# Optimization experiments

Hardware: AMD Instinct MI355X
Metric: run time of the kernel (lower is better)

Reference implementation:

```python
import jax, jax.numpy as jnp
import numpy as np

N_NODES = 50000
N_EDGES = 600000
D = 128
EDGE_DIM = 1
N_LAYERS = 2
NEG_SLOPE = 0.2


def setup_inputs() -> dict:
    key = jax.random.key(0)
    ks = jax.random.split(key, 8)
    x = jax.random.normal(ks[0], (N_NODES, D), dtype=jnp.float32)
    edge_index = jax.random.randint(ks[1], (2, N_EDGES), 0, N_NODES, dtype=jnp.int64)
    edge_attr = jax.random.normal(ks[2], (N_EDGES, EDGE_DIM), dtype=jnp.float32)
    s = 1.0 / np.sqrt(D)
    Wl = jax.random.normal(ks[3], (N_LAYERS, D, D), dtype=jnp.float32) * s   # lin_l weights
    Wr = jax.random.normal(ks[4], (N_LAYERS, D, D), dtype=jnp.float32) * s   # lin_r weights
    We = jax.random.normal(ks[5], (N_LAYERS, EDGE_DIM, D), dtype=jnp.float32) * s  # lin_edge
    att = jax.random.normal(ks[6], (N_LAYERS, D), dtype=jnp.float32) * s     # attention vector (heads=1)
    bias = jnp.zeros((N_LAYERS, D), dtype=jnp.float32)
    return {"x": x, "edge_index": edge_index, "edge_attr": edge_attr,
            "Wl": Wl, "Wr": Wr, "We": We, "att": att, "bias": bias}


def _gatv2_layer(x, src, dst, edge_attr, Wl, Wr, We, att, bias):
    # GATv2Conv, heads=1, add_self_loops=False, share_weights=False.
    xl = x @ Wl                                   # [N, D] (source transform)
    xr = x @ Wr                                   # [N, D] (target transform)
    m = xl[src] + xr[dst] + edge_attr @ We        # [E, D]
    m = jax.nn.leaky_relu(m, NEG_SLOPE)
    logits = m @ att                              # [E]
    # segment softmax over incoming edges of each dst node
    mx = jax.ops.segment_max(logits, dst, num_segments=N_NODES)  # [N]
    ex = jnp.exp(logits - mx[dst])                # [E]
    denom = jax.ops.segment_sum(ex, dst, num_segments=N_NODES)   # [N]
    alpha = ex / jnp.maximum(denom[dst], 1e-16)   # [E]
    out = jax.ops.segment_sum(alpha[:, None] * xl[src], dst, num_segments=N_NODES)
    return out + bias


def reference(x, edge_index, edge_attr, Wl, Wr, We, att, bias):
    src, dst = edge_index[0], edge_index[1]
    h = x
    for l in range(N_LAYERS):
        h = _gatv2_layer(h, src, dst, edge_attr, Wl[l], Wr[l], We[l], att[l], bias[l])
        h = jax.nn.relu(h)   # activation; norm=None, dropout=0 (eval) are identity
    return h
```

## Files before the change

### kernel.cpp

```cpp
#include <hip/hip_runtime.h>
#include <hip/hip_fp16.h>

#define N_NODES 50000
#define N_PAD   50048
#define N_EDGES 600000
#define DD 128
#define NEG_SLOPE 0.2f
#define BSHIFT 7
#define NBUCKETS 391
#define MAXB 2048

typedef _Float16 h2 __attribute__((ext_vector_type(2)));
typedef _Float16 h8 __attribute__((ext_vector_type(8)));
typedef __attribute__((ext_vector_type(4))) float f32x4;
typedef unsigned long long u64;

__device__ inline h2 bch2(unsigned u) { return __builtin_bit_cast(h2, u); }
__device__ inline unsigned h2u(h2 h) { return __builtin_bit_cast(unsigned, h); }
__device__ inline ushort f2h_bits(float x) {
    return __builtin_bit_cast(ushort, (_Float16)x);
}

#if __has_builtin(__builtin_amdgcn_fdot2)
#define DOT2(a, b, c) __builtin_amdgcn_fdot2((a), (b), (c), false)
#else
#define DOT2(a, b, c) ((c) + (float)(a)[0] * (float)(b)[0] + (float)(a)[1] * (float)(b)[1])
#endif

__global__ void pack_detect(const float* __restrict__ Wl, const float* __restrict__ Wr,
                            ushort* __restrict__ Wp,
                            const int* __restrict__ ei, int* __restrict__ flag,
                            int* __restrict__ bcount) {
    if (blockIdx.x == 256) {
        for (int t = threadIdx.x; t < NBUCKETS; t += 256) bcount[t] = 0;
        if (threadIdx.x == 0) {
            int is64 = 1;
            for (int i = 0; i < 64; ++i) {
                if (ei[2 * i + 1] != 0) { is64 = 0; break; }
            }
            *flag = is64;
        }
        return;
    }
    int idx = blockIdx.x * 256 + threadIdx.x;
    int layer = idx >> 15;
    int which = (idx >> 14) & 1;
    int kk    = (idx >> 12) & 3;
    int c     = (idx >> 9) & 7;
    int lane  = (idx >> 3) & 63;
    int j     = idx & 7;
    int k   = kk * 32 + (lane >> 4) * 8 + j;
    int col = c * 16 + (lane & 15);
    const float* W = which ? Wr : Wl;
    Wp[idx] = f2h_bits(W[(size_t)layer * DD * DD + k * DD + col]);
}

__global__ __launch_bounds__(512) void bin_edges(
    const int* __restrict__ ei, const int* __restrict__ flag,
    const float* __restrict__ ea, int* __restrict__ bcount,
    u64* __restrict__ tmp) {
    __shared__ int lhist[NBUCKETS];
    __shared__ int lbase[NBUCKETS];
    for (int i = threadIdx.x; i < NBUCKETS; i += 512) lhist[i] = 0;
    __syncthreads();
    const bool is64 = (*flag) != 0;
    int base = blockIdx.x * 4096;
    int myb[8], myrank[8];
    u64 mypack[8];
    #pragma unroll
    for (int i = 0; i < 8; ++i) {
        int e = base + i * 512 + threadIdx.x;
        if (e < N_EDGES) {
            int s, d;
            if (is64) {
                const long long* e64 = (const long long*)ei;
                s = (int)e64[e];
                d = (int)e64[N_EDGES + e];
            } else {
                s = ei[e];
                d = ei[N_EDGES + e];
            }
            unsigned hb = (unsigned)f2h_bits(ea[e]);
            int b = d >> BSHIFT;
            myb[i] = b;
            mypack[i] = ((u64)(unsigned)(d & 127) << 32) | ((u64)hb << 16) | (unsigned)s;
            myrank[i] = atomicAdd(&lhist[b], 1);
        } else myb[i] = -1;
    }
    __syncthreads();
    for (int i = threadIdx.x; i < NBUCKETS; i += 512) {
        int c = lhist[i];
        lbase[i] = c ? atomicAdd(&bcount[i], c) : 0;
    }
    __syncthreads();
    #pragma unroll
    for (int i = 0; i < 8; ++i)
        if (myb[i] >= 0) {
            int rel = lbase[myb[i]] + myrank[i];
            if (rel < MAXB)
                tmp[(size_t)myb[i] * MAXB + rel] = mypack[i];
        }
}

__global__ __launch_bounds__(256) void scatter_sort(
    const u64* __restrict__ tmp, const int* __restrict__ bcount,
    unsigned* __restrict__ se_csr, int* __restrict__ row_start) {
    __shared__ int bscan[512];
    __shared__ int lcnt[128];
    __shared__ int lscan[128];
    __shared__ int lcur[128];
    int tid = threadIdx.x;
    {
        int v = 0;
        if (tid < NBUCKETS) { v = bcount[tid]; if (v > MAXB) v = MAXB; }
        bscan[tid] = v;
        int v2 = 0;
        if (tid + 256 < NBUCKETS) { v2 = bcount[tid + 256]; if (v2 > MAXB) v2 = MAXB; }
        bscan[tid + 256] = v2;
    }
    __syncthreads();
    #pragma unroll
    for (int off = 1; off < 512; off <<= 1) {
        int t0 = (tid >= off) ? bscan[tid - off] : 0;
        int t1 = (tid + 256 >= off) ? bscan[tid + 256 - off] : 0;
        __syncthreads();
        bscan[tid] += t0;
        bscan[tid + 256] += t1;
        __syncthreads();
    }
    int b = blockIdx.x;
    int boff = (b == 0) ? 0 : bscan[b - 1];
    if (b == 0 && tid == 0) row_start[N_NODES] = bscan[NBUCKETS - 1];

    if (tid < 128) lcnt[tid] = 0;
    __syncthreads();
    int n_e = bcount[b]; if (n_e > MAXB) n_e = MAXB;
    const u64* tb = tmp + (size_t)b * MAXB;
    for (int e = tid; e < n_e; e += 256)
        atomicAdd(&lcnt[(int)(tb[e] >> 32)], 1);
    __syncthreads();
    if (tid < 128) lscan[tid] = lcnt[tid];
    __syncthreads();
    #pragma unroll
    for (int off = 1; off < 128; off <<= 1) {
        int t = 0;
        if (tid < 128 && tid >= off) t = lscan[tid - off];
        __syncthreads();
        if (tid < 128) lscan[tid] += t;
        __syncthreads();
    }
    int nb = b << BSHIFT;
    if (tid < 128) {
        int start = boff + lscan[tid] - lcnt[tid];
        lcur[tid] = start;
        if (nb + tid < N_NODES) row_start[nb + tid] = start;
    }
    __syncthreads();
    for (int e = tid; e < n_e; e += 256) {
        u64 w = tb[e];
        int pos = atomicAdd(&lcur[(int)(w >> 32)], 1);
        se_csr[pos] = (unsigned)w;
    }
}

template<bool AF32>
__global__ __launch_bounds__(256) void gemm_mfma(
    const ushort* __restrict__ h, const float* __restrict__ xf,
    const ushort* __restrict__ Wp,
    ushort* __restrict__ xl, ushort* __restrict__ xr) {
    __shared__ ushort wlds[32768];
    #pragma unroll
    for (int i = 0; i < 16; ++i) {
        int idx = i * 256 + threadIdx.x;
        ((uint4*)wlds)[idx] = ((const uint4*)Wp)[idx];
    }
    int wave = threadIdx.x >> 6, lane = threadIdx.x & 63;
    int arow = blockIdx.x * 64 + wave * 16 + (lane & 15);
    int kbase = (lane >> 4) * 8;
    f32x4 accl[8], accr[8];
    #pragma unroll
    for (int c = 0; c < 8; ++c) {
        accl[c] = (f32x4){0.f, 0.f, 0.f, 0.f};
        accr[c] = (f32x4){0.f, 0.f, 0.f, 0.f};
    }
    __syncthreads();
    #pragma unroll
    for (int kk = 0; kk < 4; ++kk) {
        h8 a;
        if (AF32) {
            if (arow < N_NODES) {
                const float* xp = xf + (size_t)arow * DD + kk * 32 + kbase;
                float4 u0 = *(const float4*)xp;
                float4 u1 = *(const float4*)(xp + 4);
                a[0] = (_Float16)u0.x; a[1] = (_Float16)u0.y;
                a[2] = (_Float16)u0.z; a[3] = (_Float16)u0.w;
                a[4] = (_Float16)u1.x; a[5] = (_Float16)u1.y;
                a[6] = (_Float16)u1.z; a[7] = (_Float16)u1.w;
            } else {
                #pragma unroll
                for (int i = 0; i < 8; ++i) a[i] = (_Float16)0.f;
            }
        } else {
            a = *(const h8*)&h[(size_t)arow * DD + kk * 32 + kbase];
        }
        #pragma unroll
        for (int c = 0; c < 8; ++c) {
            h8 bl = *(const h8*)&wlds[((kk * 8 + c) * 64 + lane) * 8];
            h8 br = *(const h8*)&wlds[16384 + ((kk * 8 + c) * 64 + lane) * 8];
            accl[c] = __builtin_amdgcn_mfma_f32_16x16x32_f16(a, bl, accl[c], 0, 0, 0);
            accr[c] = __builtin_amdgcn_mfma_f32_16x16x32_f16(a, br, accr[c], 0, 0, 0);
        }
    }
    ushort* tile = wlds;
    int drow = wave * 16 + ((lane >> 4) << 2);
    int dcol = lane & 15;
    #pragma unroll
    for (int half = 0; half < 2; ++half) {
        const f32x4* acc = half ? accr : accl;
        ushort* out = half ? xr : xl;
        __syncthreads();
        #pragma unroll
        for (int c = 0; c < 8; ++c)
            #pragma unroll
            for (int r = 0; r < 4; ++r)
                tile[(drow + r) * 136 + c * 16 + dcol] = f2h_bits(acc[c][r]);
        __syncthreads();
        #pragma unroll
        for (int it = 0; it < 8; ++it) {
            int i = it * 256 + threadIdx.x;
            int row = i >> 5, cc = (i & 31) * 4;
            int gr = blockIdx.x * 64 + row;
            if (gr < N_NODES)
                *(ushort4*)&out[(size_t)gr * DD + cc] = *(const ushort4*)&tile[row * 136 + cc];
        }
    }
}

template<bool OUT_F16>
__global__ __launch_bounds__(256, 8) void fused_node_f16(
    const ushort* __restrict__ xl, const ushort* __restrict__ xr,
    const float* __restrict__ We, const float* __restrict__ att,
    const int* __restrict__ row_start, const unsigned* __restrict__ se_csr,
    const float* __restrict__ bias, void* __restrict__ outp) {
    int wave = threadIdx.x >> 6;
    int lane = threadIdx.x & 63;
    int n = blockIdx.x * 4 + wave;
    if (n >= N_NODES) return;
    int g  = lane >> 4;
    int cb = (lane & 15) * 8;

    uint4 xrv = *(const uint4*)&xr[(size_t)n * DD + cb];
    h2 xr2[4] = {bch2(xrv.x), bch2(xrv.y), bch2(xrv.z), bch2(xrv.w)};
    float4 wf0 = *(const float4*)&We[cb], wf1 = *(const float4*)&We[cb + 4];
    float4 af0 = *(const float4*)&att[cb], af1 = *(const float4*)&att[cb + 4];
    h2 We2[4] = {{(_Float16)wf0.x, (_Float16)wf0.y}, {(_Float16)wf0.z, (_Float16)wf0.w},
                 {(_Float16)wf1.x, (_Float16)wf1.y}, {(_Float16)wf1.z, (_Float16)wf1.w}};
    h2 at2[4] = {{(_Float16)af0.x, (_Float16)af0.y}, {(_Float16)af0.z, (_Float16)af0.w},
                 {(_Float16)af1.x, (_Float16)af1.y}, {(_Float16)af1.z, (_Float16)af1.w}};
    const h2 ns2 = {(_Float16)NEG_SLOPE, (_Float16)NEG_SLOPE};

    int beg = row_start[n], end = row_start[n + 1];
    h2 acc2[4];
    #pragma unroll
    for (int k = 0; k < 4; ++k) acc2[k] = (h2){(_Float16)0.f, (_Float16)0.f};
    float denom = 0.f;

    for (int j = beg; j < end; j += 16) {
        unsigned w[4]; bool vl[4]; uint4 xv[4];
        #pragma unroll
        for (int q = 0; q < 4; ++q) {
            int e = j + 4 * q + g;
            vl[q] = e < end;
            w[q] = se_csr[vl[q] ? e : (end - 1)];
        }
        #pragma unroll
        for (int q = 0; q < 4; ++q)
            xv[q] = *(const uint4*)&xl[(size_t)(w[q] & 0xffffu) * DD + cb];
        h2 xq[4][4];
        float part[4];
        #pragma unroll
        for (int q = 0; q < 4; ++q) {
            xq[q][0] = bch2(xv[q].x); xq[q][1] = bch2(xv[q].y);
            xq[q][2] = bch2(xv[q].z); xq[q][3] = bch2(xv[q].w);
            h2 a2 = bch2((w[q] >> 16) * 0x10001u);
            float pd = 0.f;
            #pragma unroll
            for (int k = 0; k < 4; ++k) {
                h2 m = __builtin_elementwise_fma(a2, We2[k], xq[q][k] + xr2[k]);
                m = __builtin_elementwise_max(m, m * ns2);
                pd = DOT2(m, at2[k], pd);
            }
            part[q] = pd;
        }
        #pragma unroll
        for (int o = 1; o < 16; o <<= 1) {
            #pragma unroll
            for (int q = 0; q < 4; ++q) part[q] += __shfl_xor(part[q], o, 64);
        }
        #pragma unroll
        for (int q = 0; q < 4; ++q) {
            float p = vl[q] ? __expf(part[q]) : 0.f;
            denom += p;
            _Float16 ph = (_Float16)p;
            h2 p2 = {ph, ph};
            #pragma unroll
            for (int k = 0; k < 4; ++k)
                acc2[k] = __builtin_elementwise_fma(p2, xq[q][k], acc2[k]);
        }
    }

    #pragma unroll
    for (int o = 16; o < 64; o <<= 1) {
        #pragma unroll
        for (int k = 0; k < 4; ++k) {
            int t = __shfl_xor(__builtin_bit_cast(int, acc2[k]), o, 64);
            acc2[k] += __builtin_bit_cast(h2, t);
        }
        denom += __shfl_xor(denom, o, 64);
    }

    if (g == 0) {
        float inv = 1.0f / fmaxf(denom, 1e-16f);
        float o_[8];
        #pragma unroll
        for (int k = 0; k < 4; ++k) {
            o_[2 * k]     = fmaxf(fmaf((float)acc2[k][0], inv, bias[cb + 2 * k]), 0.f);
            o_[2 * k + 1] = fmaxf(fmaf((float)acc2[k][1], inv, bias[cb + 2 * k + 1]), 0.f);
        }
        if (OUT_F16) {
            uint4 o4;
            o4.x = h2u((h2){(_Float16)o_[0], (_Float16)o_[1]});
            o4.y = h2u((h2){(_Float16)o_[2], (_Float16)o_[3]});
            o4.z = h2u((h2){(_Float16)o_[4], (_Float16)o_[5]});
            o4.w = h2u((h2){(_Float16)o_[6], (_Float16)o_[7]});
            *(uint4*)((ushort*)outp + (size_t)n * DD + cb) = o4;
        } else {
            float* op = (float*)outp + (size_t)n * DD + cb;
            *(float4*)op       = *(float4*)&o_[0];
            *(float4*)(op + 4) = *(float4*)&o_[4];
        }
    }
}

extern "C" void kernel_launch(void* const* d_in, const int* in_sizes, int n_in,
                              void* d_out, int out_size, void* d_ws, size_t ws_size,
                              hipStream_t stream) {
    const float* x    = (const float*)d_in[0];
    const int*   ei   = (const int*)d_in[1];
    const float* ea   = (const float*)d_in[2];
    const float* Wl   = (const float*)d_in[3];
    const float* Wr   = (const float*)d_in[4];
    const float* We   = (const float*)d_in[5];
    const float* att  = (const float*)d_in[6];
    const float* bias = (const float*)d_in[7];

    char* wsb = (char*)d_ws;
    size_t off = 0;
    auto alloc = [&](size_t bytes) { void* r = (void*)(wsb + off); off += (bytes + 15) & ~15ull; return r; };
    ushort* h_f16    = (ushort*)alloc((size_t)N_PAD * DD * 2);
    ushort* xl_f16   = (ushort*)alloc((size_t)N_NODES * DD * 2);
    ushort* xr_f16   = (ushort*)alloc((size_t)N_NODES * DD * 2);
    ushort* Wp       = (ushort*)alloc(65536 * 2);
    u64*    tmp      = (u64*)alloc((size_t)NBUCKETS * MAXB * 8);
    unsigned* se_csr = (unsigned*)alloc((size_t)N_EDGES * 4);
    int*    row_st   = (int*)alloc((N_NODES + 1) * 4);
    int*    bcount   = (int*)alloc(NBUCKETS * 4);
    int*    flag     = (int*)alloc(4);

    pack_detect<<<257, 256, 0, stream>>>(Wl, Wr, Wp, ei, flag, bcount);

    bin_edges<<<(N_EDGES + 4095) / 4096, 512, 0, stream>>>(ei, flag, ea, bcount, tmp);
    scatter_sort<<<NBUCKETS, 256, 0, stream>>>(tmp, bcount, se_csr, row_st);

    const int ggrid = N_PAD / 64;
    for (int l = 0; l < 2; ++l) {
        const ushort* Wp_l  = Wp + (size_t)l * 32768;
        const float* We_l   = We + (size_t)l * DD;
        const float* att_l  = att + (size_t)l * DD;
        const float* bias_l = bias + (size_t)l * DD;

        if (l == 0) {
            gemm_mfma<true><<<ggrid, 256, 0, stream>>>(nullptr, x, Wp_l, xl_f16, xr_f16);
            fused_node_f16<true><<<(N_NODES + 3) / 4, 256, 0, stream>>>(
                xl_f16, xr_f16, We_l, att_l, row_st, se_csr, bias_l, (void*)h_f16);
        } else {
            gemm_mfma<false><<<ggrid, 256, 0, stream>>>(h_f16, nullptr, Wp_l, xl_f16, xr_f16);
            fused_node_f16<false><<<(N_NODES + 3) / 4, 256, 0, stream>>>(
                xl_f16, xr_f16, We_l, att_l, row_st, se_csr, bias_l, d_out);
        }
    }
}
```

Measured before the change: 123.6 us.

## Merge CSR scatter-sort and layer-0 GEMM into one heterogeneous launch

```diff
diff --git a/kernel.cpp b/kernel.cpp
--- a/kernel.cpp
+++ b/kernel.cpp
@@ -9,6 +9,7 @@
 #define BSHIFT 7
 #define NBUCKETS 391
 #define MAXB 2048
+#define GGRID (N_PAD / 64)
 
 typedef _Float16 h2 __attribute__((ext_vector_type(2)));
 typedef _Float16 h8 __attribute__((ext_vector_type(8)));
@@ -102,71 +103,139 @@
         }
 }
 
-__global__ __launch_bounds__(256) void scatter_sort(
+__global__ __launch_bounds__(256) void scatter_gemm(
     const u64* __restrict__ tmp, const int* __restrict__ bcount,
-    unsigned* __restrict__ se_csr, int* __restrict__ row_start) {
-    __shared__ int bscan[512];
-    __shared__ int lcnt[128];
-    __shared__ int lscan[128];
-    __shared__ int lcur[128];
+    unsigned* __restrict__ se_csr, int* __restrict__ row_start,
+    const float* __restrict__ xf, const ushort* __restrict__ Wp,
+    ushort* __restrict__ xl, ushort* __restrict__ xr) {
+    __shared__ ushort wlds[32768];
     int tid = threadIdx.x;
-    {
-        int v = 0;
-        if (tid < NBUCKETS) { v = bcount[tid]; if (v > MAXB) v = MAXB; }
-        bscan[tid] = v;
-        int v2 = 0;
-        if (tid + 256 < NBUCKETS) { v2 = bcount[tid + 256]; if (v2 > MAXB) v2 = MAXB; }
-        bscan[tid + 256] = v2;
+
+    if (blockIdx.x < NBUCKETS) {
+        int* bscan = (int*)wlds;
+        int* lcnt  = (int*)wlds + 512;
+        int* lscan = (int*)wlds + 640;
+        int* lcur  = (int*)wlds + 768;
+        {
+            int v = 0;
+            if (tid < NBUCKETS) { v = bcount[tid]; if (v > MAXB) v = MAXB; }
+            bscan[tid] = v;
+            int v2 = 0;
+            if (tid + 256 < NBUCKETS) { v2 = bcount[tid + 256]; if (v2 > MAXB) v2 = MAXB; }
+            bscan[tid + 256] = v2;
+        }
+        __syncthreads();
+        #pragma unroll
+        for (int off = 1; off < 512; off <<= 1) {
+            int t0 = (tid >= off) ? bscan[tid - off] : 0;
+            int t1 = (tid + 256 >= off) ? bscan[tid + 256 - off] : 0;
+            __syncthreads();
+            bscan[tid] += t0;
+            bscan[tid + 256] += t1;
+            __syncthreads();
+        }
+        int b = blockIdx.x;
+        int boff = (b == 0) ? 0 : bscan[b - 1];
+        if (b == 0 && tid == 0) row_start[N_NODES] = bscan[NBUCKETS - 1];
+
+        if (tid < 128) lcnt[tid] = 0;
+        __syncthreads();
+        int n_e = bcount[b]; if (n_e > MAXB) n_e = MAXB;
+        const u64* tb = tmp + (size_t)b * MAXB;
+        for (int e = tid; e < n_e; e += 256)
+            atomicAdd(&lcnt[(int)(tb[e] >> 32)], 1);
+        __syncthreads();
+        if (tid < 128) lscan[tid] = lcnt[tid];
+        __syncthreads();
+        #pragma unroll
+        for (int off = 1; off < 128; off <<= 1) {
+            int t = 0;
+            if (tid < 128 && tid >= off) t = lscan[tid - off];
+            __syncthreads();
+            if (tid < 128) lscan[tid] += t;
+            __syncthreads();
+        }
+        int nb = b << BSHIFT;
+        if (tid < 128) {
+            int start = boff + lscan[tid] - lcnt[tid];
+            lcur[tid] = start;
+            if (nb + tid < N_NODES) row_start[nb + tid] = start;
+        }
+        __syncthreads();
+        for (int e = tid; e < n_e; e += 256) {
+            u64 w = tb[e];
+            int pos = atomicAdd(&lcur[(int)(w >> 32)], 1);
+            se_csr[pos] = (unsigned)w;
+        }
+        return;
+    }
+
+    int bid = blockIdx.x - NBUCKETS;
+    #pragma unroll
+    for (int i = 0; i < 16; ++i) {
+        int idx = i * 256 + tid;
+        ((uint4*)wlds)[idx] = ((const uint4*)Wp)[idx];
+    }
+    int wave = tid >> 6, lane = tid & 63;
+    int arow = bid * 64 + wave * 16 + (lane & 15);
+    int kbase = (lane >> 4) * 8;
+    f32x4 accl[8], accr[8];
+    #pragma unroll
+    for (int c = 0; c < 8; ++c) {
+        accl[c] = (f32x4){0.f, 0.f, 0.f, 0.f};
+        accr[c] = (f32x4){0.f, 0.f, 0.f, 0.f};
     }
     __syncthreads();
     #pragma unroll
-    for (int off = 1; off < 512; off <<= 1) {
-        int t0 = (tid >= off) ? bscan[tid - off] : 0;
-        int t1 = (tid + 256 >= off) ? bscan[tid + 256 - off] : 0;
-        __syncthreads();
-        bscan[tid] += t0;
-        bscan[tid + 256] += t1;
-        __syncthreads();
-    }
-    int b = blockIdx.x;
-    int boff = (b == 0) ? 0 : bscan[b - 1];
-    if (b == 0 && tid == 0) row_start[N_NODES] = bscan[NBUCKETS - 1];
-
-    if (tid < 128) lcnt[tid] = 0;
-    __syncthreads();
-    int n_e = bcount[b]; if (n_e > MAXB) n_e = MAXB;
-    const u64* tb = tmp + (size_t)b * MAXB;
-    for (int e = tid; e < n_e; e += 256)
-        atomicAdd(&lcnt[(int)(tb[e] >> 32)], 1);
-    __syncthreads();
-    if (tid < 128) lscan[tid] = lcnt[tid];
-    __syncthreads();
-    #pragma unroll
-    for (int off = 1; off < 128; off <<= 1) {
-        int t = 0;
-        if (tid < 128 && tid >= off) t = lscan[tid - off];
-        __syncthreads();
-        if (tid < 128) lscan[tid] += t;
-        __syncthreads();
-    }
-    int nb = b << BSHIFT;
-    if (tid < 128) {
-        int start = boff + lscan[tid] - lcnt[tid];
-        lcur[tid] = start;
-        if (nb + tid < N_NODES) row_start[nb + tid] = start;
-    }
-    __syncthreads();
-    for (int e = tid; e < n_e; e += 256) {
-        u64 w = tb[e];
-        int pos = atomicAdd(&lcur[(int)(w >> 32)], 1);
-        se_csr[pos] = (unsigned)w;
-    }
-}
-
-template<bool AF32>
+    for (int kk = 0; kk < 4; ++kk) {
+        h8 a;
+        if (arow < N_NODES) {
+            const float* xp = xf + (size_t)arow * DD + kk * 32 + kbase;
+            float4 u0 = *(const float4*)xp;
+            float4 u1 = *(const float4*)(xp + 4);
+            a[0] = (_Float16)u0.x; a[1] = (_Float16)u0.y;
+            a[2] = (_Float16)u0.z; a[3] = (_Float16)u0.w;
+            a[4] = (_Float16)u1.x; a[5] = (_Float16)u1.y;
+            a[6] = (_Float16)u1.z; a[7] = (_Float16)u1.w;
+        } else {
+            #pragma unroll
+            for (int i = 0; i < 8; ++i) a[i] = (_Float16)0.f;
+        }
+        #pragma unroll
+        for (int c = 0; c < 8; ++c) {
+            h8 bl = *(const h8*)&wlds[((kk * 8 + c) * 64 + lane) * 8];
+            h8 br = *(const h8*)&wlds[16384 + ((kk * 8 + c) * 64 + lane) * 8];
+            accl[c] = __builtin_amdgcn_mfma_f32_16x16x32_f16(a, bl, accl[c], 0, 0, 0);
+            accr[c] = __builtin_amdgcn_mfma_f32_16x16x32_f16(a, br, accr[c], 0, 0, 0);
+        }
+    }
+    ushort* tile = wlds;
+    int drow = wave * 16 + ((lane >> 4) << 2);
+    int dcol = lane & 15;
+    #pragma unroll
+    for (int half = 0; half < 2; ++half) {
+        const f32x4* acc = half ? accr : accl;
+        ushort* out = half ? xr : xl;
+        __syncthreads();
+        #pragma unroll
+        for (int c = 0; c < 8; ++c)
+            #pragma unroll
+            for (int r = 0; r < 4; ++r)
+                tile[(drow + r) * 136 + c * 16 + dcol] = f2h_bits(acc[c][r]);
+        __syncthreads();
+        #pragma unroll
+        for (int it = 0; it < 8; ++it) {
+            int i = it * 256 + tid;
+            int row = i >> 5, cc = (i & 31) * 4;
+            int gr = bid * 64 + row;
+            if (gr < N_NODES)
+                *(ushort4*)&out[(size_t)gr * DD + cc] = *(const ushort4*)&tile[row * 136 + cc];
+        }
+    }
+}
+
 __global__ __launch_bounds__(256) void gemm_mfma(
-    const ushort* __restrict__ h, const float* __restrict__ xf,
-    const ushort* __restrict__ Wp,
+    const ushort* __restrict__ h, const ushort* __restrict__ Wp,
     ushort* __restrict__ xl, ushort* __restrict__ xr) {
     __shared__ ushort wlds[32768];
     #pragma unroll
@@ -186,23 +255,7 @@
     __syncthreads();
     #pragma unroll
     for (int kk = 0; kk < 4; ++kk) {
-        h8 a;
-        if (AF32) {
-            if (arow < N_NODES) {
-                const float* xp = xf + (size_t)arow * DD + kk * 32 + kbase;
-                float4 u0 = *(const float4*)xp;
-                float4 u1 = *(const float4*)(xp + 4);
-                a[0] = (_Float16)u0.x; a[1] = (_Float16)u0.y;
-                a[2] = (_Float16)u0.z; a[3] = (_Float16)u0.w;
-                a[4] = (_Float16)u1.x; a[5] = (_Float16)u1.y;
-                a[6] = (_Float16)u1.z; a[7] = (_Float16)u1.w;
-            } else {
-                #pragma unroll
-                for (int i = 0; i < 8; ++i) a[i] = (_Float16)0.f;
-            }
-        } else {
-            a = *(const h8*)&h[(size_t)arow * DD + kk * 32 + kbase];
-        }
+        h8 a = *(const h8*)&h[(size_t)arow * DD + kk * 32 + kbase];
         #pragma unroll
         for (int c = 0; c < 8; ++c) {
             h8 bl = *(const h8*)&wlds[((kk * 8 + c) * 64 + lane) * 8];
@@ -370,23 +423,14 @@
     pack_detect<<<257, 256, 0, stream>>>(Wl, Wr, Wp, ei, flag, bcount);
 
     bin_edges<<<(N_EDGES + 4095) / 4096, 512, 0, stream>>>(ei, flag, ea, bcount, tmp);
-    scatter_sort<<<NBUCKETS, 256, 0, stream>>>(tmp, bcount, se_csr, row_st);
-
-    const int ggrid = N_PAD / 64;
-    for (int l = 0; l < 2; ++l) {
-        const ushort* Wp_l  = Wp + (size_t)l * 32768;
-        const float* We_l   = We + (size_t)l * DD;
-        const float* att_l  = att + (size_t)l * DD;
-        const float* bias_l = bias + (size_t)l * DD;
-
-        if (l == 0) {
-            gemm_mfma<true><<<ggrid, 256, 0, stream>>>(nullptr, x, Wp_l, xl_f16, xr_f16);
-            fused_node_f16<true><<<(N_NODES + 3) / 4, 256, 0, stream>>>(
-                xl_f16, xr_f16, We_l, att_l, row_st, se_csr, bias_l, (void*)h_f16);
-        } else {
-            gemm_mfma<false><<<ggrid, 256, 0, stream>>>(h_f16, nullptr, Wp_l, xl_f16, xr_f16);
-            fused_node_f16<false><<<(N_NODES + 3) / 4, 256, 0, stream>>>(
-                xl_f16, xr_f16, We_l, att_l, row_st, se_csr, bias_l, d_out);
-        }
-    }
-}
+
+    scatter_gemm<<<NBUCKETS + GGRID, 256, 0, stream>>>(
+        tmp, bcount, se_csr, row_st, x, Wp, xl_f16, xr_f16);
+
+    fused_node_f16<true><<<(N_NODES + 3) / 4, 256, 0, stream>>>(
+        xl_f16, xr_f16, We, att, row_st, se_csr, bias, (void*)h_f16);
+
+    gemm_mfma<<<GGRID, 256, 0, stream>>>(h_f16, Wp + 32768, xl_f16, xr_f16);
+    fused_node_f16<false><<<(N_NODES + 3) / 4, 256, 0, stream>>>(
+        xl_f16, xr_f16, We + DD, att + DD, row_st, se_csr, bias + DD, d_out);
+}
```

Measured after the change: 119.9 us (median of 2 runs). 3.0% less time.
